# Performance work log

Measured on AMD Instinct MI355X. Metric: run time of the kernel, lower is better.

## Reference

```python
import jax, jax.numpy as jnp
import numpy as np

ALPHA, BETA, GAMMA = 1.0, 0.5, 0.3
EPS = 1e-08


def setup_inputs() -> dict:
    key = jax.random.key(0)
    k1, k2, k3, k4, k5 = jax.random.split(key, 5)
    B, C, F = 32, 256, 2048
    return {
        "mag_hat": jax.random.normal(k1, (B, C, F), dtype=jnp.float32),
        "phase_hat": jax.random.normal(k2, (B, C, F), dtype=jnp.float32),
        "mag_target": jax.random.normal(k3, (B, C, F), dtype=jnp.float32),
        "phase_target": jax.random.normal(k4, (B, C, F), dtype=jnp.float32),
        "pci_target": jax.random.uniform(k5, (B, C, C), dtype=jnp.float32),
    }


def _pci(phase):
    # phase: (B, C, F). Naive form is mean_f cos/sin(phi_i - phi_j) over a
    # (B,C,C,F) broadcast; rewrite with cos(a-b)=ca*cb+sa*sb and
    # sin(a-b)=sa*cb-ca*sb as two batched GEMMs on (C,F) matrices.
    c = jnp.cos(phase)
    s = jnp.sin(phase)
    inv_f = 1.0 / phase.shape[-1]
    real = (jnp.einsum('bif,bjf->bij', c, c) + jnp.einsum('bif,bjf->bij', s, s)) * inv_f
    imag = (jnp.einsum('bif,bjf->bij', s, c) - jnp.einsum('bif,bjf->bij', c, s)) * inv_f
    return jnp.sqrt(real * real + imag * imag + EPS)


def reference(mag_hat, phase_hat, mag_target, phase_target, pci_target):
    mag_loss = jnp.mean((mag_hat - mag_target) ** 2)
    phase_loss = jnp.mean(1.0 - jnp.cos(phase_hat - phase_target))
    pci_hat = _pci(phase_hat)
    coh_loss = jnp.mean((pci_hat - pci_target) ** 2)
    total = ALPHA * mag_loss + BETA * phase_loss + GAMMA * coh_loss
    return (total, mag_loss, phase_loss, coh_loss)
```

## Files before the change

kernel.cpp:

```cpp
#include <hip/hip_runtime.h>
#include <hip/hip_bf16.h>

#define ALPHA_ 1.0f
#define BETA_  0.5f
#define GAMMA_ 0.3f
#define EPS_   1e-8f

typedef unsigned short u16;

constexpr int B_ = 32, C_ = 256, F_ = 2048;
constexpr int NTOT = B_ * C_ * F_;
constexpr int N4   = NTOT / 4;
constexpr int NCC  = B_ * C_ * C_;

typedef __bf16 bf16x8 __attribute__((ext_vector_type(8)));
typedef float  f32x4  __attribute__((ext_vector_type(4)));

__device__ __forceinline__ u16 f2bf(float x) {
    unsigned u = __float_as_uint(x);
    u += 0x7fffu + ((u >> 16) & 1u);
    return (u16)(u >> 16);
}

__global__ void __launch_bounds__(256)
ew_kernel(const float4* __restrict__ mh, const float4* __restrict__ ph,
          const float4* __restrict__ mt, const float4* __restrict__ pt,
          short4* __restrict__ cb, short4* __restrict__ sb,
          float* __restrict__ accum)
{
    __shared__ float sm[4], sp[4];
    int tid    = blockIdx.x * 256 + threadIdx.x;
    int stride = gridDim.x * 256;
    float msum = 0.f, psum = 0.f;

    for (int i = tid; i < N4; i += stride) {
        float4 a = mh[i], b = mt[i];
        float dx = a.x - b.x, dy = a.y - b.y, dz = a.z - b.z, dw = a.w - b.w;
        msum += dx * dx + dy * dy + dz * dz + dw * dw;

        float4 p = ph[i], q = pt[i];
        psum += 4.f - __cosf(p.x - q.x) - __cosf(p.y - q.y)
                    - __cosf(p.z - q.z) - __cosf(p.w - q.w);

        float sx, cx, sy, cy, sz, cz, sw, cw;
        __sincosf(p.x, &sx, &cx);
        __sincosf(p.y, &sy, &cy);
        __sincosf(p.z, &sz, &cz);
        __sincosf(p.w, &sw, &cw);
        cb[i] = make_short4((short)f2bf(cx), (short)f2bf(cy),
                            (short)f2bf(cz), (short)f2bf(cw));
        sb[i] = make_short4((short)f2bf(sx), (short)f2bf(sy),
                            (short)f2bf(sz), (short)f2bf(sw));
    }

    #pragma unroll
    for (int o = 32; o > 0; o >>= 1) {
        msum += __shfl_down(msum, o, 64);
        psum += __shfl_down(psum, o, 64);
    }
    int lane = threadIdx.x & 63, wv = threadIdx.x >> 6;
    if (lane == 0) { sm[wv] = msum; sp[wv] = psum; }
    __syncthreads();
    if (threadIdx.x == 0) {
        atomicAdd(&accum[0], sm[0] + sm[1] + sm[2] + sm[3]);
        atomicAdd(&accum[1], sp[0] + sp[1] + sp[2] + sp[3]);
    }
}

#define LDA 40

__global__ void __launch_bounds__(256)
pci_kernel(const u16* __restrict__ cb, const u16* __restrict__ sb,
           const float* __restrict__ tgt, float* __restrict__ accum)
{
    __shared__ u16 lac[64 * LDA], las[64 * LDA];
    __shared__ u16 lbc[64 * LDA], lbs[64 * LDA];
    __shared__ float sred[4];

    const int b  = blockIdx.y;
    const int ti = blockIdx.x >> 2, tj = blockIdx.x & 3;
    const int i0 = ti * 64, j0 = tj * 64;

    const int t    = threadIdx.x;
    const int lane = t & 63, wv = t >> 6;
    const int wrow = (wv >> 1) * 32, wcol = (wv & 1) * 32;
    const int m = lane & 15, q = lane >> 4;

    const int srow = t >> 2;
    const int sk   = (t & 3) << 3;
    const size_t bbase = (size_t)b * (C_ * F_);
    const size_t ga = bbase + (size_t)(i0 + srow) * F_ + sk;
    const size_t gb = bbase + (size_t)(j0 + srow) * F_ + sk;
    const int ldst = srow * LDA + sk;

    f32x4 zero = {0.f, 0.f, 0.f, 0.f};
    f32x4 accR[2][2], accSC[2][2], accCS[2][2];
    #pragma unroll
    for (int a = 0; a < 2; a++)
        #pragma unroll
        for (int c = 0; c < 2; c++) {
            accR[a][c] = zero; accSC[a][c] = zero; accCS[a][c] = zero;
        }

    for (int k0 = 0; k0 < F_; k0 += 32) {
        __syncthreads();
        *(int4*)&lac[ldst] = *(const int4*)&cb[ga + k0];
        *(int4*)&las[ldst] = *(const int4*)&sb[ga + k0];
        *(int4*)&lbc[ldst] = *(const int4*)&cb[gb + k0];
        *(int4*)&lbs[ldst] = *(const int4*)&sb[gb + k0];
        __syncthreads();

        bf16x8 fac[2], fas[2], fbc[2], fbs[2];
        #pragma unroll
        for (int a = 0; a < 2; a++) {
            int r = (wrow + a * 16 + m) * LDA + q * 8;
            fac[a] = *(const bf16x8*)&lac[r];
            fas[a] = *(const bf16x8*)&las[r];
        }
        #pragma unroll
        for (int c = 0; c < 2; c++) {
            int r = (wcol + c * 16 + m) * LDA + q * 8;
            fbc[c] = *(const bf16x8*)&lbc[r];
            fbs[c] = *(const bf16x8*)&lbs[r];
        }

        #pragma unroll
        for (int a = 0; a < 2; a++)
            #pragma unroll
            for (int c = 0; c < 2; c++) {
                accR[a][c]  = __builtin_amdgcn_mfma_f32_16x16x32_bf16(fac[a], fbc[c], accR[a][c], 0, 0, 0);
                accR[a][c]  = __builtin_amdgcn_mfma_f32_16x16x32_bf16(fas[a], fbs[c], accR[a][c], 0, 0, 0);
                accSC[a][c] = __builtin_amdgcn_mfma_f32_16x16x32_bf16(fas[a], fbc[c], accSC[a][c], 0, 0, 0);
                accCS[a][c] = __builtin_amdgcn_mfma_f32_16x16x32_bf16(fac[a], fbs[c], accCS[a][c], 0, 0, 0);
            }
    }

    const float inv_f = 1.0f / (float)F_;
    float coh = 0.f;
    const float* tb = tgt + (size_t)b * (C_ * C_);
    #pragma unroll
    for (int a = 0; a < 2; a++)
        #pragma unroll
        for (int c = 0; c < 2; c++) {
            int irow = i0 + wrow + a * 16 + q * 4;
            int jcol = j0 + wcol + c * 16 + m;
            #pragma unroll
            for (int r = 0; r < 4; r++) {
                float re = accR[a][c][r] * inv_f;
                float im = (accSC[a][c][r] - accCS[a][c][r]) * inv_f;
                float p  = sqrtf(re * re + im * im + EPS_);
                float d  = p - tb[(irow + r) * C_ + jcol];
                coh += d * d;
            }
        }

    #pragma unroll
    for (int o = 32; o > 0; o >>= 1) coh += __shfl_down(coh, o, 64);
    if (lane == 0) sred[wv] = coh;
    __syncthreads();
    if (t == 0) atomicAdd(&accum[2], sred[0] + sred[1] + sred[2] + sred[3]);
}

__global__ void fin_kernel(const float* __restrict__ accum, float* __restrict__ out)
{
    if (threadIdx.x == 0) {
        float mag = accum[0] * (1.0f / (float)NTOT);
        float phs = accum[1] * (1.0f / (float)NTOT);
        float coh = accum[2] * (1.0f / (float)NCC);
        out[0] = ALPHA_ * mag + BETA_ * phs + GAMMA_ * coh;
        out[1] = mag;
        out[2] = phs;
        out[3] = coh;
    }
}

extern "C" void kernel_launch(void* const* d_in, const int* in_sizes, int n_in,
                              void* d_out, int out_size, void* d_ws, size_t ws_size,
                              hipStream_t stream)
{
    const float* mh  = (const float*)d_in[0];
    const float* ph  = (const float*)d_in[1];
    const float* mt  = (const float*)d_in[2];
    const float* pt  = (const float*)d_in[3];
    const float* tgt = (const float*)d_in[4];
    float* out = (float*)d_out;

    float* accum = (float*)d_ws;
    u16* cb = (u16*)((char*)d_ws + 256);
    u16* sb = cb + (size_t)NTOT;

    hipMemsetAsync(d_ws, 0, 16, stream);

    ew_kernel<<<2048, 256, 0, stream>>>(
        (const float4*)mh, (const float4*)ph, (const float4*)mt, (const float4*)pt,
        (short4*)cb, (short4*)sb, accum);

    dim3 grid(16, 32);
    pci_kernel<<<grid, 256, 0, stream>>>(cb, sb, tgt, accum);

    fin_kernel<<<1, 64, 0, stream>>>(accum, out);
}
```

Before: 324.9 us.

## Interleave cos/sin bf16 workspace and register-prefetch larger K tiles in PCI GEMM

The elementwise kernel now handles 8 elements per thread and writes cos and sin as interleaved 16-byte chunks into one workspace, so each row carries 8 cos values followed by 8 sin values. The PCI kernel stages 128-wide K tiles through padded LDS and prefetches the next tile from global memory into registers while the MFMAs run. It also uses a 1D grid whose remapping spreads tiles of a batch across blocks, and sets launch_bounds to 2 blocks per SM. The aim is fewer syncs per K, overlap of global loads with compute, and better cache locality. In exchange it uses more registers and a larger LDS footprint.

```diff
diff --git a/kernel.cpp b/kernel.cpp
--- a/kernel.cpp
+++ b/kernel.cpp
@@ -7,10 +7,11 @@
 #define EPS_   1e-8f
 
 typedef unsigned short u16;
+typedef unsigned int u32;
 
 constexpr int B_ = 32, C_ = 256, F_ = 2048;
 constexpr int NTOT = B_ * C_ * F_;
-constexpr int N4   = NTOT / 4;
+constexpr int G8   = NTOT / 8;
 constexpr int NCC  = B_ * C_ * C_;
 
 typedef __bf16 bf16x8 __attribute__((ext_vector_type(8)));
@@ -25,32 +26,43 @@
 __global__ void __launch_bounds__(256)
 ew_kernel(const float4* __restrict__ mh, const float4* __restrict__ ph,
           const float4* __restrict__ mt, const float4* __restrict__ pt,
-          short4* __restrict__ cb, short4* __restrict__ sb,
-          float* __restrict__ accum)
+          int4* __restrict__ W, float* __restrict__ accum)
 {
     __shared__ float sm[4], sp[4];
     int tid    = blockIdx.x * 256 + threadIdx.x;
     int stride = gridDim.x * 256;
     float msum = 0.f, psum = 0.f;
 
-    for (int i = tid; i < N4; i += stride) {
-        float4 a = mh[i], b = mt[i];
-        float dx = a.x - b.x, dy = a.y - b.y, dz = a.z - b.z, dw = a.w - b.w;
-        msum += dx * dx + dy * dy + dz * dz + dw * dw;
-
-        float4 p = ph[i], q = pt[i];
-        psum += 4.f - __cosf(p.x - q.x) - __cosf(p.y - q.y)
-                    - __cosf(p.z - q.z) - __cosf(p.w - q.w);
-
-        float sx, cx, sy, cy, sz, cz, sw, cw;
-        __sincosf(p.x, &sx, &cx);
-        __sincosf(p.y, &sy, &cy);
-        __sincosf(p.z, &sz, &cz);
-        __sincosf(p.w, &sw, &cw);
-        cb[i] = make_short4((short)f2bf(cx), (short)f2bf(cy),
-                            (short)f2bf(cz), (short)f2bf(cw));
-        sb[i] = make_short4((short)f2bf(sx), (short)f2bf(sy),
-                            (short)f2bf(sz), (short)f2bf(sw));
+    #pragma unroll 2
+    for (int g = tid; g < G8; g += stride) {
+        float4 p0 = ph[2 * g], p1 = ph[2 * g + 1];
+        float4 q0 = pt[2 * g], q1 = pt[2 * g + 1];
+        float4 a0 = mh[2 * g], a1 = mh[2 * g + 1];
+        float4 b0 = mt[2 * g], b1 = mt[2 * g + 1];
+
+        float pv[8] = {p0.x, p0.y, p0.z, p0.w, p1.x, p1.y, p1.z, p1.w};
+        float qv[8] = {q0.x, q0.y, q0.z, q0.w, q1.x, q1.y, q1.z, q1.w};
+        float av[8] = {a0.x, a0.y, a0.z, a0.w, a1.x, a1.y, a1.z, a1.w};
+        float bv[8] = {b0.x, b0.y, b0.z, b0.w, b1.x, b1.y, b1.z, b1.w};
+
+        u32 cu[8], su[8];
+        #pragma unroll
+        for (int j = 0; j < 8; j++) {
+            float dm = av[j] - bv[j];
+            msum += dm * dm;
+            psum += 1.f - __cosf(pv[j] - qv[j]);
+            float s, c;
+            __sincosf(pv[j], &s, &c);
+            cu[j] = f2bf(c);
+            su[j] = f2bf(s);
+        }
+        int4 cv = make_int4((int)(cu[0] | (cu[1] << 16)), (int)(cu[2] | (cu[3] << 16)),
+                            (int)(cu[4] | (cu[5] << 16)), (int)(cu[6] | (cu[7] << 16)));
+        int4 sv = make_int4((int)(su[0] | (su[1] << 16)), (int)(su[2] | (su[3] << 16)),
+                            (int)(su[4] | (su[5] << 16)), (int)(su[6] | (su[7] << 16)));
+        int4* dst = W + (size_t)g * 2;
+        dst[0] = cv;
+        dst[1] = sv;
     }
 
     #pragma unroll
@@ -67,18 +79,23 @@
     }
 }
 
-#define LDA 40
-
-__global__ void __launch_bounds__(256)
-pci_kernel(const u16* __restrict__ cb, const u16* __restrict__ sb,
-           const float* __restrict__ tgt, float* __restrict__ accum)
-{
-    __shared__ u16 lac[64 * LDA], las[64 * LDA];
-    __shared__ u16 lbc[64 * LDA], lbs[64 * LDA];
+#define LSTR 272
+
+__global__ void __launch_bounds__(256, 2)
+pci_kernel(const u16* __restrict__ Wg, const float* __restrict__ tgt,
+           float* __restrict__ accum)
+{
+    __shared__ int4 la4[64 * 17];
+    __shared__ int4 lb4[64 * 17];
     __shared__ float sred[4];
-
-    const int b  = blockIdx.y;
-    const int ti = blockIdx.x >> 2, tj = blockIdx.x & 3;
+    char* la = (char*)la4;
+    char* lb = (char*)lb4;
+
+    const int g  = blockIdx.x;
+    const int x  = g & 7, sq = g >> 3;
+    const int y  = (x << 2) | (sq & 3);
+    const int tt = sq >> 2;
+    const int ti = tt >> 2, tj = tt & 3;
     const int i0 = ti * 64, j0 = tj * 64;
 
     const int t    = threadIdx.x;
@@ -86,12 +103,17 @@
     const int wrow = (wv >> 1) * 32, wcol = (wv & 1) * 32;
     const int m = lane & 15, q = lane >> 4;
 
-    const int srow = t >> 2;
-    const int sk   = (t & 3) << 3;
-    const size_t bbase = (size_t)b * (C_ * F_);
-    const size_t ga = bbase + (size_t)(i0 + srow) * F_ + sk;
-    const size_t gb = bbase + (size_t)(j0 + srow) * F_ + sk;
-    const int ldst = srow * LDA + sk;
+    const int srow = t >> 4;
+    const int scol = (t & 15) * 16;
+    const char* Ab = (const char*)Wg + ((size_t)y * 256 + i0) * 8192;
+    const char* Bb = (const char*)Wg + ((size_t)y * 256 + j0) * 8192;
+
+    int4 pa[4], pb[4];
+    #pragma unroll
+    for (int r = 0; r < 4; r++) {
+        pa[r] = *(const int4*)(Ab + (size_t)(srow + r * 16) * 8192 + scol);
+        pb[r] = *(const int4*)(Bb + (size_t)(srow + r * 16) * 8192 + scol);
+    }
 
     f32x4 zero = {0.f, 0.f, 0.f, 0.f};
     f32x4 accR[2][2], accSC[2][2], accCS[2][2];
@@ -102,42 +124,54 @@
             accR[a][c] = zero; accSC[a][c] = zero; accCS[a][c] = zero;
         }
 
-    for (int k0 = 0; k0 < F_; k0 += 32) {
+    for (int it = 0; it < 32; ++it) {
         __syncthreads();
-        *(int4*)&lac[ldst] = *(const int4*)&cb[ga + k0];
-        *(int4*)&las[ldst] = *(const int4*)&sb[ga + k0];
-        *(int4*)&lbc[ldst] = *(const int4*)&cb[gb + k0];
-        *(int4*)&lbs[ldst] = *(const int4*)&sb[gb + k0];
+        #pragma unroll
+        for (int r = 0; r < 4; r++) {
+            *(int4*)(la + (srow + r * 16) * LSTR + scol) = pa[r];
+            *(int4*)(lb + (srow + r * 16) * LSTR + scol) = pb[r];
+        }
         __syncthreads();
 
-        bf16x8 fac[2], fas[2], fbc[2], fbs[2];
-        #pragma unroll
-        for (int a = 0; a < 2; a++) {
-            int r = (wrow + a * 16 + m) * LDA + q * 8;
-            fac[a] = *(const bf16x8*)&lac[r];
-            fas[a] = *(const bf16x8*)&las[r];
-        }
-        #pragma unroll
-        for (int c = 0; c < 2; c++) {
-            int r = (wcol + c * 16 + m) * LDA + q * 8;
-            fbc[c] = *(const bf16x8*)&lbc[r];
-            fbs[c] = *(const bf16x8*)&lbs[r];
-        }
-
-        #pragma unroll
-        for (int a = 0; a < 2; a++)
+        if (it < 31) {
+            const int koff = (it + 1) * 256;
+            #pragma unroll
+            for (int r = 0; r < 4; r++) {
+                pa[r] = *(const int4*)(Ab + (size_t)(srow + r * 16) * 8192 + koff + scol);
+                pb[r] = *(const int4*)(Bb + (size_t)(srow + r * 16) * 8192 + koff + scol);
+            }
+        }
+
+        #pragma unroll
+        for (int s = 0; s < 2; ++s) {
+            bf16x8 fac[2], fas[2], fbc[2], fbs[2];
+            #pragma unroll
+            for (int a = 0; a < 2; a++) {
+                const char* p = la + (wrow + a * 16 + m) * LSTR + s * 128 + q * 32;
+                fac[a] = *(const bf16x8*)p;
+                fas[a] = *(const bf16x8*)(p + 16);
+            }
             #pragma unroll
             for (int c = 0; c < 2; c++) {
-                accR[a][c]  = __builtin_amdgcn_mfma_f32_16x16x32_bf16(fac[a], fbc[c], accR[a][c], 0, 0, 0);
-                accR[a][c]  = __builtin_amdgcn_mfma_f32_16x16x32_bf16(fas[a], fbs[c], accR[a][c], 0, 0, 0);
-                accSC[a][c] = __builtin_amdgcn_mfma_f32_16x16x32_bf16(fas[a], fbc[c], accSC[a][c], 0, 0, 0);
-                accCS[a][c] = __builtin_amdgcn_mfma_f32_16x16x32_bf16(fac[a], fbs[c], accCS[a][c], 0, 0, 0);
-            }
+                const char* p = lb + (wcol + c * 16 + m) * LSTR + s * 128 + q * 32;
+                fbc[c] = *(const bf16x8*)p;
+                fbs[c] = *(const bf16x8*)(p + 16);
+            }
+            #pragma unroll
+            for (int a = 0; a < 2; a++)
+                #pragma unroll
+                for (int c = 0; c < 2; c++) {
+                    accR[a][c]  = __builtin_amdgcn_mfma_f32_16x16x32_bf16(fac[a], fbc[c], accR[a][c], 0, 0, 0);
+                    accR[a][c]  = __builtin_amdgcn_mfma_f32_16x16x32_bf16(fas[a], fbs[c], accR[a][c], 0, 0, 0);
+                    accSC[a][c] = __builtin_amdgcn_mfma_f32_16x16x32_bf16(fas[a], fbc[c], accSC[a][c], 0, 0, 0);
+                    accCS[a][c] = __builtin_amdgcn_mfma_f32_16x16x32_bf16(fac[a], fbs[c], accCS[a][c], 0, 0, 0);
+                }
+        }
     }
 
     const float inv_f = 1.0f / (float)F_;
     float coh = 0.f;
-    const float* tb = tgt + (size_t)b * (C_ * C_);
+    const float* tb = tgt + (size_t)y * (C_ * C_);
     #pragma unroll
     for (int a = 0; a < 2; a++)
         #pragma unroll
@@ -186,17 +220,15 @@
     float* out = (float*)d_out;
 
     float* accum = (float*)d_ws;
-    u16* cb = (u16*)((char*)d_ws + 256);
-    u16* sb = cb + (size_t)NTOT;
+    int4* W = (int4*)((char*)d_ws + 256);
 
     hipMemsetAsync(d_ws, 0, 16, stream);
 
     ew_kernel<<<2048, 256, 0, stream>>>(
         (const float4*)mh, (const float4*)ph, (const float4*)mt, (const float4*)pt,
-        (short4*)cb, (short4*)sb, accum);
-
-    dim3 grid(16, 32);
-    pci_kernel<<<grid, 256, 0, stream>>>(cb, sb, tgt, accum);
+        W, accum);
+
+    pci_kernel<<<512, 256, 0, stream>>>((const u16*)W, tgt, accum);
 
     fin_kernel<<<1, 64, 0, stream>>>(accum, out);
 }
```

Measured after the change: 444.5 us. 1.37x slower.
